# Kernel optimization log

Measured on AMD Instinct MI355X. Metric: run time of the kernel, lower is better.

The kernel has to match this reference:

```python
import jax, jax.numpy as jnp
import numpy as np

B, T, E = 4, 2048, 1024
H = 16
QK_SQUEEZE = 2
S = E // QK_SQUEEZE          # squeeze_dim = 512
SHD = S // H                 # squeeze_head_dim = 32
HD = E // H                  # head_dim = 64
SCALING = SHD ** -0.5


def setup_inputs() -> dict:
    key = jax.random.key(0)
    ks = jax.random.split(key, 9)
    def w(k, shape, fan_in):
        return jax.random.normal(k, shape, jnp.float32) * (fan_in ** -0.5)
    return {
        "hidden_states": jax.random.normal(ks[0], (B, T, E), jnp.float32),
        "Wq": w(ks[1], (E, S), E), "bq": jnp.zeros((S,), jnp.float32),
        "Wk": w(ks[2], (E, S), E), "bk": jnp.zeros((S,), jnp.float32),
        "Wv": w(ks[3], (E, E), E), "bv": jnp.zeros((E,), jnp.float32),
        "Wo": w(ks[4], (E, E), E), "bo": jnp.zeros((E,), jnp.float32),
    }


def reference(hidden_states, Wq, bq, Wk, bk, Wv, bv, Wo, bo):
    # Projections; Q pre-scaled as in the torch module.
    q = ((hidden_states @ Wq + bq) * SCALING).reshape(B, T, H, SHD)
    k = (hidden_states @ Wk + bk).reshape(B, T, H, SHD)
    v = (hidden_states @ Wv + bv).reshape(B, T, H, HD)
    # [B, H, Tq, Tk] attention logits with squeezed head dim.
    attn = jnp.einsum("bqhd,bkhd->bhqk", q, k)
    p = jax.nn.softmax(attn, axis=-1)  # dropout p=0.0 -> identity
    out = jnp.einsum("bhqk,bkhd->bqhd", p, v).reshape(B, T, E)
    return out @ Wo + bo
```

## Files before the change

kernel.cpp:

```cpp
#include <hip/hip_runtime.h>
#include <stdint.h>


#define QSCALE (0.17677669529663687f * 1.4426950408889634f)

typedef __bf16 bf16x8 __attribute__((ext_vector_type(8)));
typedef float f32x4 __attribute__((ext_vector_type(4)));
typedef float f32x8 __attribute__((ext_vector_type(8)));
typedef float f32x16 __attribute__((ext_vector_type(16)));
typedef unsigned int u32x2 __attribute__((ext_vector_type(2)));
typedef unsigned int u32x4v __attribute__((ext_vector_type(4)));

static __device__ __forceinline__ unsigned short f2b(float f) {
  return __builtin_bit_cast(unsigned short, (__bf16)f);
}
static __device__ __forceinline__ unsigned int cvtpk(float lo, float hi) {
  unsigned int r;
  asm("v_cvt_pk_bf16_f32 %0, %1, %2" : "=v"(r) : "v"(lo), "v"(hi));
  return r;
}
static __device__ __forceinline__ void gl_lds16(const void* g, void* s) {
  __builtin_amdgcn_global_load_lds(
      (const __attribute__((address_space(1))) unsigned int*)(uintptr_t)g,
      (__attribute__((address_space(3))) unsigned int*)(uintptr_t)s, 16, 0, 0);
}
static __device__ __forceinline__ void pswap(unsigned int& a, unsigned int& b) {
#if __has_builtin(__builtin_amdgcn_permlane32_swap)
  u32x2 r = __builtin_amdgcn_permlane32_swap(a, b, false, false);
  a = r.x;
  b = r.y;
#else
  asm("v_permlane32_swap_b32 %0, %1" : "+v"(a), "+v"(b));
#endif
}

__global__ void k_cvt_hs(const float* __restrict__ in, unsigned short* __restrict__ out) {
  int i = (blockIdx.x * 256 + threadIdx.x) * 4;
  float4 v = *(const float4*)(in + i);
  ushort4 u = make_ushort4(f2b(v.x), f2b(v.y), f2b(v.z), f2b(v.w));
  *(ushort4*)(out + i) = u;
}

__global__ void k_cvt_wT(const float* __restrict__ W, unsigned short* __restrict__ WT,
                         int N, float scale) {
  __shared__ float tile[64][65];
  const int kt = blockIdx.x & 15;
  const int nt = blockIdx.x >> 4;
  const int k0 = kt * 64, n0 = nt * 64;
  const int t = threadIdx.x;
  {
    int kl = t >> 2, c = t & 3;
    const float* src = W + (size_t)(k0 + kl) * N + n0 + c * 16;
#pragma unroll
    for (int j = 0; j < 4; j++) {
      float4 v = *(const float4*)(src + j * 4);
      tile[kl][c * 16 + j * 4 + 0] = v.x;
      tile[kl][c * 16 + j * 4 + 1] = v.y;
      tile[kl][c * 16 + j * 4 + 2] = v.z;
      tile[kl][c * 16 + j * 4 + 3] = v.w;
    }
  }
  __syncthreads();
  {
    int nl = t >> 2, c2 = t & 3;
    unsigned short us[16];
#pragma unroll
    for (int j = 0; j < 16; j++) us[j] = f2b(tile[c2 * 16 + j][nl] * scale);
    uint4 a, b;
    a.x = (unsigned)us[0] | ((unsigned)us[1] << 16);
    a.y = (unsigned)us[2] | ((unsigned)us[3] << 16);
    a.z = (unsigned)us[4] | ((unsigned)us[5] << 16);
    a.w = (unsigned)us[6] | ((unsigned)us[7] << 16);
    b.x = (unsigned)us[8] | ((unsigned)us[9] << 16);
    b.y = (unsigned)us[10] | ((unsigned)us[11] << 16);
    b.z = (unsigned)us[12] | ((unsigned)us[13] << 16);
    b.w = (unsigned)us[14] | ((unsigned)us[15] << 16);
    unsigned short* dst = WT + (size_t)(n0 + nl) * 1024 + k0 + c2 * 16;
    *(uint4*)dst = a;
    *(uint4*)(dst + 8) = b;
  }
}

__global__ void k_bias(const float* __restrict__ bq, const float* __restrict__ bk,
                       const float* __restrict__ bv, float* __restrict__ bqkv) {
  int n = blockIdx.x * 256 + threadIdx.x;
  float v;
  if (n < 512) v = bq[n] * QSCALE;
  else if (n < 1024) v = bk[n - 512];
  else v = bv[n - 1024];
  bqkv[n] = v;
}

__global__ __launch_bounds__(512, 2) void k_gemm256qkv(
    const unsigned short* __restrict__ A, const unsigned short* __restrict__ BT,
    const float* __restrict__ bias,
    unsigned short* __restrict__ qo, unsigned short* __restrict__ ko,
    unsigned short* __restrict__ vo) {
  __shared__ alignas(128) char smem[131072];
  const int tid = threadIdx.x;
  const int w = tid >> 6, l = tid & 63, lm = l & 15, lc = l >> 4;
  const int wm = w >> 2, wn = w & 3;
  const int mt = blockIdx.x & 31, nt = blockIdx.x >> 5;
  const int brow = mt << 8, bcol = nt << 8;

  f32x4 acc[8][4] = {};

  auto stage = [&](int kt, int buf) {
    const unsigned short* As = A + (size_t)brow * 1024 + kt * 64;
    const unsigned short* Bs = BT + (size_t)bcol * 1024 + kt * 64;
    char* la = smem + buf * 32768;
    char* lb = smem + 65536 + buf * 32768;
#pragma unroll
    for (int j = 0; j < 4; j++) {
      const int p = j * 512 + tid;
      gl_lds16(As + (size_t)(p >> 3) * 1024 + (p & 7) * 8, la + (j * 512 + w * 64) * 16);
      gl_lds16(Bs + (size_t)(p >> 3) * 1024 + (p & 7) * 8, lb + (j * 512 + w * 64) * 16);
    }
  };

  auto phase = [&](const char* la, const char* lb, int mg, int ng) {
    bf16x8 af[4][2], bf[2][2];
#pragma unroll
    for (int mi = 0; mi < 4; mi++)
#pragma unroll
      for (int kk = 0; kk < 2; kk++)
        af[mi][kk] = *(const bf16x8*)(la + (wm * 128 + (mg + mi) * 16 + lm) * 128 +
                                      kk * 64 + lc * 16);
#pragma unroll
    for (int ni = 0; ni < 2; ni++)
#pragma unroll
      for (int kk = 0; kk < 2; kk++)
        bf[ni][kk] = *(const bf16x8*)(lb + (wn * 64 + (ng + ni) * 16 + lm) * 128 +
                                      kk * 64 + lc * 16);
    __builtin_amdgcn_s_setprio(1);
#pragma unroll
    for (int mi = 0; mi < 4; mi++)
#pragma unroll
      for (int ni = 0; ni < 2; ni++)
#pragma unroll
        for (int kk = 0; kk < 2; kk++)
          acc[mg + mi][ng + ni] = __builtin_amdgcn_mfma_f32_16x16x32_bf16(
              af[mi][kk], bf[ni][kk], acc[mg + mi][ng + ni], 0, 0, 0);
    __builtin_amdgcn_s_setprio(0);
    __builtin_amdgcn_sched_barrier(0);
  };

  auto ktile = [&](int buf) {
    const char* la = smem + buf * 32768;
    const char* lb = smem + 65536 + buf * 32768;
    phase(la, lb, 0, 0);
    phase(la, lb, 4, 0);
    phase(la, lb, 0, 2);
    phase(la, lb, 4, 2);
  };

  stage(0, 0);
  __syncthreads();
#pragma unroll 1
  for (int kt2 = 0; kt2 < 8; kt2++) {
    if (kt2 * 2 + 1 < 16) stage(kt2 * 2 + 1, 1);
    ktile(0);
    __syncthreads();
    if (kt2 * 2 + 2 < 16) stage(kt2 * 2 + 2, 0);
    ktile(1);
    __syncthreads();
  }

#pragma unroll
  for (int nf = 0; nf < 4; nf++) {
    const int n = bcol + wn * 64 + nf * 16 + lm;
    const float bv_ = bias[n];
#pragma unroll
    for (int mf = 0; mf < 8; mf++) {
      const int m0 = brow + wm * 128 + mf * 16 + lc * 4;
      f32x4 v = acc[mf][nf];
      const float x0 = v[0] + bv_, x1 = v[1] + bv_, x2 = v[2] + bv_, x3 = v[3] + bv_;
      const int b = m0 >> 11, t0 = m0 & 2047;
      if (n < 1024) {
        unsigned short* dst = (n < 512) ? qo : ko;
        const int nn = n & 511, h = nn >> 5, d = nn & 31;
        const size_t base = ((size_t)((b << 4) + h) * 2048 + t0) * 32 + d;
        dst[base + 0 * 32] = f2b(x0);
        dst[base + 1 * 32] = f2b(x1);
        dst[base + 2 * 32] = f2b(x2);
        dst[base + 3 * 32] = f2b(x3);
      } else {
        const int e = n - 1024, h = e >> 6, hd = e & 63;
        ushort4 u = make_ushort4(f2b(x0), f2b(x1), f2b(x2), f2b(x3));
        *(ushort4*)(vo + (((size_t)((b << 4) + h) * 256 + (t0 >> 3)) * 64 + hd) * 8 +
                    (t0 & 7)) = u;
      }
    }
  }
}

template <int MODE>
__global__ __launch_bounds__(256) void k_gemm(
    const unsigned short* __restrict__ A, const unsigned short* __restrict__ BT,
    const float* __restrict__ bias, int M, int N,
    unsigned short* __restrict__ qo, unsigned short* __restrict__ ko,
    unsigned short* __restrict__ vo, float* __restrict__ fo) {
  constexpr int K = 1024;
  __shared__ alignas(128) char smem[16384];
  const int tid = threadIdx.x;
  const int w = tid >> 6, l = tid & 63, lm = l & 15, lc = l >> 4;
  const int nmt = M >> 7;
  const int mt = blockIdx.x % nmt, nt = blockIdx.x / nmt;
  const int brow = mt << 7, bcol = nt << 7;
  const int wm = w >> 1, wn = w & 1;
  f32x4 acc[4][4] = {};
  const int ca = w * 64 + l;

  for (int k0 = 0; k0 < K; k0 += 32) {
#pragma unroll
    for (int j = 0; j < 2; j++) {
      int c = j * 256 + ca;
      gl_lds16(A + (size_t)(brow + (c >> 2)) * K + k0 + (c & 3) * 8,
               smem + (j * 256 + w * 64) * 16);
      gl_lds16(BT + (size_t)(bcol + (c >> 2)) * K + k0 + (c & 3) * 8,
               smem + 8192 + (j * 256 + w * 64) * 16);
    }
    __syncthreads();
    bf16x8 af[4], bf[4];
#pragma unroll
    for (int i = 0; i < 4; i++) {
      af[i] = *(const bf16x8*)(smem + (wm * 64 + i * 16 + lm) * 64 + lc * 16);
      bf[i] = *(const bf16x8*)(smem + 8192 + (wn * 64 + i * 16 + lm) * 64 + lc * 16);
    }
#pragma unroll
    for (int ai = 0; ai < 4; ai++)
#pragma unroll
      for (int bj = 0; bj < 4; bj++)
        acc[ai][bj] = __builtin_amdgcn_mfma_f32_16x16x32_bf16(af[ai], bf[bj], acc[ai][bj], 0, 0, 0);
    __syncthreads();
  }

#pragma unroll
  for (int bj = 0; bj < 4; bj++) {
    const int n = bcol + wn * 64 + bj * 16 + lm;
    const float bv_ = bias[n];
#pragma unroll
    for (int ai = 0; ai < 4; ai++) {
      const int m0 = brow + wm * 64 + ai * 16 + lc * 4;
      f32x4 v = acc[ai][bj];
      const float x0 = v[0] + bv_, x1 = v[1] + bv_, x2 = v[2] + bv_, x3 = v[3] + bv_;
      if constexpr (MODE == 0) {
        const int b = m0 >> 11, t0 = m0 & 2047;
        if (n < 1024) {
          unsigned short* dst = (n < 512) ? qo : ko;
          const int nn = n & 511, h = nn >> 5, d = nn & 31;
          const size_t base = ((size_t)((b << 4) + h) * 2048 + t0) * 32 + d;
          dst[base + 0 * 32] = f2b(x0);
          dst[base + 1 * 32] = f2b(x1);
          dst[base + 2 * 32] = f2b(x2);
          dst[base + 3 * 32] = f2b(x3);
        } else {
          const int e = n - 1024, h = e >> 6, hd = e & 63;
          ushort4 u = make_ushort4(f2b(x0), f2b(x1), f2b(x2), f2b(x3));
          *(ushort4*)(vo + (((size_t)((b << 4) + h) * 256 + (t0 >> 3)) * 64 + hd) * 8 +
                      (t0 & 7)) = u;
        }
      } else {
        float* dst = fo + (size_t)m0 * N + n;
        dst[0 * N] = x0;
        dst[1 * N] = x1;
        dst[2 * N] = x2;
        dst[3 * N] = x3;
      }
    }
  }
}

__global__ __launch_bounds__(128, 2) void k_attn6(
    const unsigned short* __restrict__ qb, const unsigned short* __restrict__ kb,
    const unsigned short* __restrict__ v3, unsigned short* __restrict__ aout) {
  __shared__ float red[64][67];
  const int tid = threadIdx.x, kvh = tid >> 6, l = tid & 63;
  const int l31 = l & 31, hf = l >> 5;
  const int xcd = blockIdx.x & 7, slot = blockIdx.x >> 3;
  const int bh = xcd + ((slot >> 5) << 3);
  const int qrow0 = (slot & 31) << 6;

  const unsigned short* qrow = qb + ((size_t)bh * 2048 + qrow0 + l31) * 32 + hf * 8;
  const bf16x8 qA0 = *(const bf16x8*)(qrow);
  const bf16x8 qA1 = *(const bf16x8*)(qrow + 16);
  const bf16x8 qB0 = *(const bf16x8*)(qrow + 1024);
  const bf16x8 qB1 = *(const bf16x8*)(qrow + 1024 + 16);

  const unsigned short* kp = kb + ((size_t)bh * 2048 + kvh * 1024 + l31) * 32 + hf * 8;
  const unsigned short* vp = v3 + (((size_t)bh * 256 + kvh * 128 + hf) * 64 + l31) * 8;

  f32x16 oA0 = {}, oA1 = {}, oB0 = {}, oB1 = {};
  f32x4 lsA4 = {}, lsB4 = {};

  auto tile_body = [&](bf16x8 kf0, bf16x8 kf1, bf16x8 va00, bf16x8 va01, bf16x8 va10,
                       bf16x8 va11) {
    f32x16 sA = {}, sB = {};
    sA = __builtin_amdgcn_mfma_f32_32x32x16_bf16(kf0, qA0, sA, 0, 0, 0);
    sA = __builtin_amdgcn_mfma_f32_32x32x16_bf16(kf1, qA1, sA, 0, 0, 0);
    sB = __builtin_amdgcn_mfma_f32_32x32x16_bf16(kf0, qB0, sB, 0, 0, 0);
    sB = __builtin_amdgcn_mfma_f32_32x32x16_bf16(kf1, qB1, sB, 0, 0, 0);

#pragma unroll
    for (int i = 0; i < 16; i++) sA[i] = __builtin_amdgcn_exp2f(sA[i]);
#pragma unroll
    for (int i = 0; i < 16; i++) sB[i] = __builtin_amdgcn_exp2f(sB[i]);
    {
      f32x8 t8 = __builtin_shufflevector(sA, sA, 0, 1, 2, 3, 4, 5, 6, 7) +
                 __builtin_shufflevector(sA, sA, 8, 9, 10, 11, 12, 13, 14, 15);
      lsA4 += __builtin_shufflevector(t8, t8, 0, 1, 2, 3) +
              __builtin_shufflevector(t8, t8, 4, 5, 6, 7);
    }
    {
      f32x8 t8 = __builtin_shufflevector(sB, sB, 0, 1, 2, 3, 4, 5, 6, 7) +
                 __builtin_shufflevector(sB, sB, 8, 9, 10, 11, 12, 13, 14, 15);
      lsB4 += __builtin_shufflevector(t8, t8, 0, 1, 2, 3) +
              __builtin_shufflevector(t8, t8, 4, 5, 6, 7);
    }
    unsigned int pa[8], pb[8];
#pragma unroll
    for (int i = 0; i < 8; i++) pa[i] = cvtpk(sA[2 * i], sA[2 * i + 1]);
#pragma unroll
    for (int i = 0; i < 8; i++) pb[i] = cvtpk(sB[2 * i], sB[2 * i + 1]);
    pswap(pa[0], pa[2]);
    pswap(pa[1], pa[3]);
    pswap(pa[4], pa[6]);
    pswap(pa[5], pa[7]);
    pswap(pb[0], pb[2]);
    pswap(pb[1], pb[3]);
    pswap(pb[4], pb[6]);
    pswap(pb[5], pb[7]);
    const bf16x8 fA0 = __builtin_bit_cast(bf16x8, (u32x4v){pa[0], pa[1], pa[2], pa[3]});
    const bf16x8 fA1 = __builtin_bit_cast(bf16x8, (u32x4v){pa[4], pa[5], pa[6], pa[7]});
    const bf16x8 fB0 = __builtin_bit_cast(bf16x8, (u32x4v){pb[0], pb[1], pb[2], pb[3]});
    const bf16x8 fB1 = __builtin_bit_cast(bf16x8, (u32x4v){pb[4], pb[5], pb[6], pb[7]});

    __builtin_amdgcn_s_setprio(1);
    oA0 = __builtin_amdgcn_mfma_f32_32x32x16_bf16(va00, fA0, oA0, 0, 0, 0);
    oA1 = __builtin_amdgcn_mfma_f32_32x32x16_bf16(va01, fA0, oA1, 0, 0, 0);
    oB0 = __builtin_amdgcn_mfma_f32_32x32x16_bf16(va00, fB0, oB0, 0, 0, 0);
    oB1 = __builtin_amdgcn_mfma_f32_32x32x16_bf16(va01, fB0, oB1, 0, 0, 0);
    oA0 = __builtin_amdgcn_mfma_f32_32x32x16_bf16(va10, fA1, oA0, 0, 0, 0);
    oA1 = __builtin_amdgcn_mfma_f32_32x32x16_bf16(va11, fA1, oA1, 0, 0, 0);
    oB0 = __builtin_amdgcn_mfma_f32_32x32x16_bf16(va10, fB1, oB0, 0, 0, 0);
    oB1 = __builtin_amdgcn_mfma_f32_32x32x16_bf16(va11, fB1, oB1, 0, 0, 0);
    __builtin_amdgcn_s_setprio(0);
  };

  bf16x8 kf0 = *(const bf16x8*)(kp);
  bf16x8 kf1 = *(const bf16x8*)(kp + 16);
  bf16x8 va00 = *(const bf16x8*)(vp + 0);
  bf16x8 va01 = *(const bf16x8*)(vp + 256);
  bf16x8 va10 = *(const bf16x8*)(vp + 1024);
  bf16x8 va11 = *(const bf16x8*)(vp + 1280);

  for (int it = 0; it < 31; ++it) {
    kp += 1024;
    vp += 2048;
    const bf16x8 nk0 = *(const bf16x8*)(kp);
    const bf16x8 nk1 = *(const bf16x8*)(kp + 16);
    const bf16x8 nv00 = *(const bf16x8*)(vp + 0);
    const bf16x8 nv01 = *(const bf16x8*)(vp + 256);
    const bf16x8 nv10 = *(const bf16x8*)(vp + 1024);
    const bf16x8 nv11 = *(const bf16x8*)(vp + 1280);

    tile_body(kf0, kf1, va00, va01, va10, va11);

    kf0 = nk0;
    kf1 = nk1;
    va00 = nv00;
    va01 = nv01;
    va10 = nv10;
    va11 = nv11;
  }
  tile_body(kf0, kf1, va00, va01, va10, va11);

  float lsA = (lsA4[0] + lsA4[1]) + (lsA4[2] + lsA4[3]);
  float lsB = (lsB4[0] + lsB4[1]) + (lsB4[2] + lsB4[3]);
  lsA += __shfl_xor(lsA, 32);
  lsB += __shfl_xor(lsB, 32);

  if (kvh == 1) {
    float* r = &red[l][0];
#pragma unroll
    for (int i = 0; i < 16; i++) {
      r[i] = oA0[i];
      r[16 + i] = oA1[i];
      r[32 + i] = oB0[i];
      r[48 + i] = oB1[i];
    }
    r[64] = lsA;
    r[65] = lsB;
  }
  __syncthreads();
  if (kvh == 0) {
    const float* r = &red[l][0];
#pragma unroll
    for (int i = 0; i < 16; i++) {
      oA0[i] += r[i];
      oA1[i] += r[16 + i];
      oB0[i] += r[32 + i];
      oB1[i] += r[48 + i];
    }
    lsA += r[64];
    lsB += r[65];

    const int b = bh >> 4, hh = bh & 15;
    const float rA = 1.0f / lsA, rB = 1.0f / lsB;
    unsigned short* orowA = aout + ((size_t)(b * 2048 + qrow0 + l31)) * 1024 + hh * 64;
    unsigned short* orowB = orowA + (size_t)32 * 1024;
#pragma unroll
    for (int hc = 0; hc < 2; hc++) {
#pragma unroll
      for (int rg = 0; rg < 4; rg++) {
        const f32x16& oa = hc ? oA1 : oA0;
        ushort4 ua = make_ushort4(f2b(oa[rg * 4 + 0] * rA), f2b(oa[rg * 4 + 1] * rA),
                                  f2b(oa[rg * 4 + 2] * rA), f2b(oa[rg * 4 + 3] * rA));
        *(ushort4*)(orowA + hc * 32 + rg * 8 + hf * 4) = ua;
        const f32x16& ob = hc ? oB1 : oB0;
        ushort4 ub = make_ushort4(f2b(ob[rg * 4 + 0] * rB), f2b(ob[rg * 4 + 1] * rB),
                                  f2b(ob[rg * 4 + 2] * rB), f2b(ob[rg * 4 + 3] * rB));
        *(ushort4*)(orowB + hc * 32 + rg * 8 + hf * 4) = ub;
      }
    }
  }
}

extern "C" void kernel_launch(void* const* d_in, const int* in_sizes, int n_in,
                              void* d_out, int out_size, void* d_ws, size_t ws_size,
                              hipStream_t stream) {
  const float* hs = (const float*)d_in[0];
  const float* Wq = (const float*)d_in[1];
  const float* bq = (const float*)d_in[2];
  const float* Wk = (const float*)d_in[3];
  const float* bk = (const float*)d_in[4];
  const float* Wv = (const float*)d_in[5];
  const float* bv = (const float*)d_in[6];
  const float* Wo = (const float*)d_in[7];
  const float* bo = (const float*)d_in[8];

  char* ws = (char*)d_ws;
  unsigned short* hsb   = (unsigned short*)(ws + 0);
  unsigned short* wqkvT = (unsigned short*)(ws + 16777216);
  unsigned short* woT   = (unsigned short*)(ws + 20971520);
  float*          bqkv  = (float*)        (ws + 23068672);
  unsigned short* qbuf  = (unsigned short*)(ws + 23076864);
  unsigned short* kbuf  = (unsigned short*)(ws + 31465472);
  unsigned short* vTb   = (unsigned short*)(ws + 39854080);
  unsigned short* aoutb = (unsigned short*)(ws + 56631296);

  k_cvt_hs<<<8192, 256, 0, stream>>>(hs, hsb);
  k_cvt_wT<<<128, 256, 0, stream>>>(Wq, wqkvT, 512, QSCALE);
  k_cvt_wT<<<128, 256, 0, stream>>>(Wk, wqkvT + 512 * 1024, 512, 1.0f);
  k_cvt_wT<<<256, 256, 0, stream>>>(Wv, wqkvT + 1024 * 1024, 1024, 1.0f);
  k_cvt_wT<<<256, 256, 0, stream>>>(Wo, woT, 1024, 1.0f);
  k_bias<<<8, 256, 0, stream>>>(bq, bk, bv, bqkv);

  k_gemm256qkv<<<256, 512, 0, stream>>>(hsb, wqkvT, bqkv, qbuf, kbuf, vTb);
  k_attn6<<<2048, 128, 0, stream>>>(qbuf, kbuf, vTb, aoutb);
  k_gemm<1><<<64 * 8, 256, 0, stream>>>(aoutb, woT, bo, 8192, 1024,
                                        nullptr, nullptr, nullptr, (float*)d_out);
}
```

Before: 173.4 us.

## XOR-swizzle LDS tiles and deepen QKV GEMM prefetch to two stages ahead

Applies an XOR swizzle to the column chunk when staging A/B tiles into LDS and undoes it on the fragment reads, aiming to remove LDS bank conflicts. The K loop is restructured so two tiles are in flight, with explicit vmcnt waits and raw s_barriers in place of __syncthreads. Each k-subtile now loads all 8x4 fragments and issues 32 MFMAs at once. This raises register pressure and relies on hand-placed waitcnt counts being correct.

```diff
diff --git a/kernel.cpp b/kernel.cpp
--- a/kernel.cpp
+++ b/kernel.cpp
@@ -113,57 +113,55 @@
 #pragma unroll
     for (int j = 0; j < 4; j++) {
       const int p = j * 512 + tid;
-      gl_lds16(As + (size_t)(p >> 3) * 1024 + (p & 7) * 8, la + (j * 512 + w * 64) * 16);
-      gl_lds16(Bs + (size_t)(p >> 3) * 1024 + (p & 7) * 8, lb + (j * 512 + w * 64) * 16);
+      const int r = p >> 3;
+      const int cc = (p & 7) ^ (r & 7);
+      gl_lds16(As + (size_t)r * 1024 + cc * 8, la + (j * 512 + w * 64) * 16);
+      gl_lds16(Bs + (size_t)r * 1024 + cc * 8, lb + (j * 512 + w * 64) * 16);
     }
   };
 
-  auto phase = [&](const char* la, const char* lb, int mg, int ng) {
-    bf16x8 af[4][2], bf[2][2];
-#pragma unroll
-    for (int mi = 0; mi < 4; mi++)
-#pragma unroll
-      for (int kk = 0; kk < 2; kk++)
-        af[mi][kk] = *(const bf16x8*)(la + (wm * 128 + (mg + mi) * 16 + lm) * 128 +
-                                      kk * 64 + lc * 16);
-#pragma unroll
-    for (int ni = 0; ni < 2; ni++)
-#pragma unroll
-      for (int kk = 0; kk < 2; kk++)
-        bf[ni][kk] = *(const bf16x8*)(lb + (wn * 64 + (ng + ni) * 16 + lm) * 128 +
-                                      kk * 64 + lc * 16);
-    __builtin_amdgcn_s_setprio(1);
-#pragma unroll
-    for (int mi = 0; mi < 4; mi++)
-#pragma unroll
-      for (int ni = 0; ni < 2; ni++)
-#pragma unroll
-        for (int kk = 0; kk < 2; kk++)
-          acc[mg + mi][ng + ni] = __builtin_amdgcn_mfma_f32_16x16x32_bf16(
-              af[mi][kk], bf[ni][kk], acc[mg + mi][ng + ni], 0, 0, 0);
-    __builtin_amdgcn_s_setprio(0);
+  stage(0, 0);
+  stage(1, 1);
+  asm volatile("s_waitcnt vmcnt(8)" ::: "memory");
+  __builtin_amdgcn_s_barrier();
+  __builtin_amdgcn_sched_barrier(0);
+
+#pragma unroll 2
+  for (int t = 0; t < 16; ++t) {
+    const char* la = smem + (t & 1) * 32768;
+    const char* lb = smem + 65536 + (t & 1) * 32768;
+#pragma unroll
+    for (int kk = 0; kk < 2; kk++) {
+      const int csw = kk * 64 + lc * 16;
+      bf16x8 af[8], bf[4];
+#pragma unroll
+      for (int mi = 0; mi < 8; mi++)
+        af[mi] = *(const bf16x8*)(la + (wm * 128 + mi * 16 + lm) * 128 +
+                                  (csw ^ ((lm & 7) << 4)));
+#pragma unroll
+      for (int ni = 0; ni < 4; ni++)
+        bf[ni] = *(const bf16x8*)(lb + (wn * 64 + ni * 16 + lm) * 128 +
+                                  (csw ^ ((lm & 7) << 4)));
+      __builtin_amdgcn_s_setprio(1);
+#pragma unroll
+      for (int mi = 0; mi < 8; mi++)
+#pragma unroll
+        for (int ni = 0; ni < 4; ni++)
+          acc[mi][ni] = __builtin_amdgcn_mfma_f32_16x16x32_bf16(af[mi], bf[ni],
+                                                                acc[mi][ni], 0, 0, 0);
+      __builtin_amdgcn_s_setprio(0);
+    }
+    asm volatile("s_waitcnt lgkmcnt(0)" ::: "memory");
     __builtin_amdgcn_sched_barrier(0);
-  };
-
-  auto ktile = [&](int buf) {
-    const char* la = smem + buf * 32768;
-    const char* lb = smem + 65536 + buf * 32768;
-    phase(la, lb, 0, 0);
-    phase(la, lb, 4, 0);
-    phase(la, lb, 0, 2);
-    phase(la, lb, 4, 2);
-  };
-
-  stage(0, 0);
-  __syncthreads();
-#pragma unroll 1
-  for (int kt2 = 0; kt2 < 8; kt2++) {
-    if (kt2 * 2 + 1 < 16) stage(kt2 * 2 + 1, 1);
-    ktile(0);
-    __syncthreads();
-    if (kt2 * 2 + 2 < 16) stage(kt2 * 2 + 2, 0);
-    ktile(1);
-    __syncthreads();
+    __builtin_amdgcn_s_barrier();
+    if (t + 2 < 16) {
+      stage(t + 2, t & 1);
+      asm volatile("s_waitcnt vmcnt(8)" ::: "memory");
+    } else {
+      asm volatile("s_waitcnt vmcnt(0)" ::: "memory");
+    }
+    __builtin_amdgcn_s_barrier();
+    __builtin_amdgcn_sched_barrier(0);
   }
 
 #pragma unroll
```

New measurement: 154.7 us. 1.12x faster.
